# Optimization experiments

Measured on AMD Instinct MI355X. Metric: run time of the kernel, lower is better.

## Reference

```python
import jax, jax.numpy as jnp
import numpy as np

TEMP = 0.1

def _normalized_grid(B, H, W, dtype=jnp.float32):
    # normalized coords in [-1, 1], (x, y) order, shape [B, H, W, 2]
    ys = jnp.linspace(-1.0, 1.0, H, dtype=dtype)
    xs = jnp.linspace(-1.0, 1.0, W, dtype=dtype)
    gy, gx = jnp.meshgrid(ys, xs, indexing='ij')
    grid = jnp.stack([gx, gy], axis=-1)  # [H, W, 2]
    return jnp.broadcast_to(grid, (B, H, W, 2))


def setup_inputs() -> dict:
    key = jax.random.key(0)
    k1, k2, k3 = jax.random.split(key, 3)
    B, H, W, D = 8, 48, 48, 1024
    f_mv_A = jax.random.normal(k1, (B, H, W, D), dtype=jnp.float32)
    f_mv_B = jax.random.normal(k2, (B, H, W, D), dtype=jnp.float32)
    # omega buffer: 2*pi*randn(dim//2, 2)
    omega = 2.0 * jnp.pi * jax.random.normal(k3, (D // 2, 2), dtype=jnp.float32)
    scale = jnp.ones((), dtype=jnp.float32)
    return {"f_mv_A": f_mv_A, "f_mv_B": f_mv_B, "omega": omega, "scale": scale}


def reference(f_mv_A, f_mv_B, omega, scale):
    B, H_A, W_A, D = f_mv_A.shape
    _, H_B, W_B, _ = f_mv_B.shape
    # Fourier positional embedding grid over image B coordinates
    x = _normalized_grid(B, H_B, W_B).reshape(B, H_B * W_B, 2)
    x_emb = x @ (scale * omega).T                      # [B, HW_B, D//2]
    pos_emb_grid = jnp.concatenate([jnp.sin(x_emb), jnp.cos(x_emb)], axis=-1)  # [B, HW_B, D]

    # cosine similarity cross-attention
    fa = f_mv_A / jnp.linalg.norm(f_mv_A, axis=-1, keepdims=True)
    fb = f_mv_B / jnp.linalg.norm(f_mv_B, axis=-1, keepdims=True)
    fa = fa.reshape(B, H_A * W_A, D)
    fb = fb.reshape(B, H_B * W_B, D)
    attn_logits = (1.0 / TEMP) * jnp.einsum('bqd,bkd->bqk', fa, fb)  # [B, HW_A, HW_B]
    attn = jax.nn.softmax(attn_logits, axis=2)
    match_emb = jnp.einsum('bqk,bkd->bqd', attn, pos_emb_grid)        # [B, HW_A, D]

    attn_logits = attn_logits.reshape(B, H_A, W_A, H_B, W_B)
    attn = attn.reshape(B, H_A, W_A, H_B, W_B)
    match_emb = match_emb.reshape(B, H_A, W_A, D)
    return attn_logits, attn, match_emb
```

## Files before the change

### kernel.cpp

```cpp
#include <hip/hip_runtime.h>
#include <stdint.h>
#include <math.h>

#define NBATCH 8
#define HWSZ   2304
#define DDIM   1024
#define NROWS  (NBATCH*HWSZ)
#define PLANE  ((size_t)NROWS*DDIM)
#define OFF1   ((size_t)NBATCH*HWSZ*HWSZ)
#define OFF2   (2*OFF1)

typedef __attribute__((ext_vector_type(8))) short bf16x8;
typedef __attribute__((ext_vector_type(8))) _Float16 f16x8;
typedef __attribute__((ext_vector_type(4))) float f32x4;

#define GLOAD16(g, l) __builtin_amdgcn_global_load_lds( \
    (const __attribute__((address_space(1))) void*)(g), \
    (__attribute__((address_space(3))) void*)(l), 16, 0, 0)

__device__ __forceinline__ float bf2f(uint16_t u) {
    union { uint32_t i; float f; } v; v.i = ((uint32_t)u) << 16; return v.f;
}
__device__ __forceinline__ uint16_t f2bf(float f) {
    union { uint32_t i; float f; } v; v.f = f;
    uint32_t x = v.i;
    return (uint16_t)((x + 0x7fffu + ((x >> 16) & 1u)) >> 16);
}
__device__ __forceinline__ float h2f(uint16_t u) {
    _Float16 h; __builtin_memcpy(&h, &u, 2); return (float)h;
}
__device__ __forceinline__ uint16_t f2h(float f) {
    _Float16 h = (_Float16)f; uint16_t u; __builtin_memcpy(&u, &h, 2); return u;
}
__device__ __forceinline__ int dmode(const uint16_t* s) {
    uint16_t v = s[0];
    return (v == 0x3F80u) ? 1 : ((v == 0x3C00u) ? 2 : 0);
}
__device__ __forceinline__ float dec16(uint16_t u, int m) { return (m == 1) ? bf2f(u) : h2f(u); }
__device__ __forceinline__ uint16_t enc16(float f, int m) { return (m == 1) ? f2bf(f) : f2h(f); }

__global__ void prep_kernel(const void* __restrict__ inA, const void* __restrict__ inB,
                            const void* __restrict__ omega, const uint16_t* __restrict__ scalep,
                            float* __restrict__ rn, uint16_t* __restrict__ posT,
                            int* __restrict__ rowT, int* __restrict__ colT,
                            void* __restrict__ outbase) {
    const int mode = dmode(scalep);
    int g = blockIdx.x;
    int t = threadIdx.x;
    if (g == 0) {
        if (t < 64) {
            int lane = t;
            int m = lane & 15, q = lane >> 4;
            bf16x8 a1, b1, a2, b2;
            #pragma unroll
            for (int j = 0; j < 8; j++) {
                int k = q * 8 + j;
                float k0 = (k == 0) ? 1.0f : 0.0f;
                a1[j] = (short)f2bf(k0);
                b1[j] = (short)f2bf(k0 * (float)(m + 1));
                a2[j] = (short)f2bf(k0 * (float)(m + 1));
                b2[j] = (short)f2bf(k0);
            }
            f32x4 z = {0.f, 0.f, 0.f, 0.f};
            f32x4 d1 = __builtin_amdgcn_mfma_f32_16x16x32_bf16(a1, b1, z, 0, 0, 0);
            f32x4 d2 = __builtin_amdgcn_mfma_f32_16x16x32_bf16(a2, b2, z, 0, 0, 0);
            #pragma unroll
            for (int r = 0; r < 4; r++) {
                colT[lane * 4 + r] = (int)d1[r] - 1;
                rowT[lane * 4 + r] = (int)d2[r] - 1;
            }
        }
        return;
    }
    if (g <= 512) {
        int j = g - 1;
        float om0, om1, sc;
        if (mode == 0) {
            const float* om = (const float*)omega;
            om0 = om[j * 2]; om1 = om[j * 2 + 1];
            sc = *(const float*)scalep;
        } else {
            const uint16_t* om = (const uint16_t*)omega;
            om0 = dec16(om[j * 2], mode); om1 = dec16(om[j * 2 + 1], mode);
            sc = dec16(scalep[0], mode);
        }
        om0 *= sc; om1 *= sc;
        for (int p = t; p < HWSZ; p += 256) {
            int iy = p / 48, ix = p % 48;
            float gx = (2.0f / 47.0f) * (float)ix - 1.0f;
            float gy = (2.0f / 47.0f) * (float)iy - 1.0f;
            float e = om0 * gx + om1 * gy;
            size_t chunk = (size_t)(p >> 5) * (DDIM * 32);
            int kin = p & 31;
            posT[chunk + (size_t)j * 32 + kin]           = f2bf(sinf(e));
            posT[chunk + (size_t)(j + 512) * 32 + kin]   = f2bf(cosf(e));
        }
        return;
    }
    int row = g - 513;
    const void* src = (row < NROWS) ? inA : inB;
    int lrow = (row < NROWS) ? row : row - NROWS;
    float v[4];
    if (mode == 0) {
        const float* p = (const float*)src + (size_t)lrow * DDIM + t * 4;
        float4 f = *(const float4*)p;
        v[0] = f.x; v[1] = f.y; v[2] = f.z; v[3] = f.w;
        uint16_t* hbase = (uint16_t*)((float*)outbase + OFF1) + ((row < NROWS) ? 0 : PLANE);
        uint16_t h0 = f2h(v[0]), h1 = f2h(v[1]), h2 = f2h(v[2]), h3 = f2h(v[3]);
        uint2 hv;
        hv.x = (uint32_t)h0 | ((uint32_t)h1 << 16);
        hv.y = (uint32_t)h2 | ((uint32_t)h3 << 16);
        *(uint2*)(hbase + (size_t)lrow * DDIM + t * 4) = hv;
    } else {
        const uint16_t* p = (const uint16_t*)src + (size_t)lrow * DDIM + t * 4;
        uint2 u = *(const uint2*)p;
        v[0] = dec16(u.x & 0xffff, mode); v[1] = dec16(u.x >> 16, mode);
        v[2] = dec16(u.y & 0xffff, mode); v[3] = dec16(u.y >> 16, mode);
    }
    float ss = v[0]*v[0] + v[1]*v[1] + v[2]*v[2] + v[3]*v[3];
    __shared__ float red[256];
    red[t] = ss; __syncthreads();
    for (int s = 128; s > 0; s >>= 1) { if (t < s) red[t] += red[t + s]; __syncthreads(); }
    if (t == 0) rn[row] = 1.0f / sqrtf(red[0]);
}

__launch_bounds__(256, 2)
__global__ void gemm1_mfma(const void* __restrict__ inA, const void* __restrict__ inB,
                           const uint16_t* __restrict__ scalep, const float* __restrict__ rn,
                           void* __restrict__ outbase,
                           const int* __restrict__ rowT, const int* __restrict__ colT) {
    const int mode = dmode(scalep);
    __shared__ uint16_t sA[128 * 32];
    __shared__ uint16_t sB[128 * 32];
    __shared__ float rnS[256];
    int g = blockIdx.x;
    int swz = (g & 7) * 324 + (g >> 3);
    int b = swz / 324;
    int rr = swz % 324;
    int tm = rr / 18, tn = rr % 18;
    int t = threadIdx.x;
    if (t < 128) rnS[t] = 10.0f * rn[(size_t)b * HWSZ + tm * 128 + t];
    else         rnS[t] = rn[(size_t)NROWS + (size_t)b * HWSZ + tn * 128 + (t - 128)];
    int lane = t & 63, wave = t >> 6;
    int wm = (wave & 1) * 64, wn = (wave >> 1) * 64;
    int lr = lane & 15, ko = (lane >> 4) * 8;
    size_t rowA0 = (size_t)b * HWSZ + tm * 128;
    size_t rowB0 = (size_t)b * HWSZ + tn * 128;
    const uint16_t* pA16;
    const uint16_t* pB16;
    if (mode == 0) {
        const uint16_t* planes = (const uint16_t*)((const float*)outbase + OFF1);
        pA16 = planes + rowA0 * DDIM;
        pB16 = planes + PLANE + rowB0 * DDIM;
    } else {
        pA16 = (const uint16_t*)inA + rowA0 * DDIM;
        pB16 = (const uint16_t*)inB + rowB0 * DDIM;
    }
    int srow = wave * 32 + (lane >> 2);
    int squart = (lane & 3) * 8;
    const uint16_t* aS0 = pA16 + (size_t)srow * DDIM + squart;
    const uint16_t* aS1 = aS0 + (size_t)16 * DDIM;
    const uint16_t* bS0 = pB16 + (size_t)srow * DDIM + squart;
    const uint16_t* bS1 = bS0 + (size_t)16 * DDIM;
    uint16_t* aD0 = sA + (wave * 32) * 32;
    uint16_t* aD1 = aD0 + 512;
    uint16_t* bD0 = sB + (wave * 32) * 32;
    uint16_t* bD1 = bD0 + 512;
    f32x4 acc[4][4] = {};

    for (int k0 = 0; k0 < DDIM; k0 += 32) {
        __syncthreads();
        GLOAD16(aS0 + k0, aD0);
        GLOAD16(aS1 + k0, aD1);
        GLOAD16(bS0 + k0, bD0);
        GLOAD16(bS1 + k0, bD1);
        __syncthreads();
        if (mode == 1) {
            bf16x8 af[4], bf_[4];
            #pragma unroll
            for (int i = 0; i < 4; i++) af[i] = *(const bf16x8*)(sA + (wm + i * 16 + lr) * 32 + ko);
            #pragma unroll
            for (int j = 0; j < 4; j++) bf_[j] = *(const bf16x8*)(sB + (wn + j * 16 + lr) * 32 + ko);
            #pragma unroll
            for (int i = 0; i < 4; i++)
                #pragma unroll
                for (int j = 0; j < 4; j++)
                    acc[i][j] = __builtin_amdgcn_mfma_f32_16x16x32_bf16(af[i], bf_[j], acc[i][j], 0, 0, 0);
        } else {
            f16x8 af[4], bf_[4];
            #pragma unroll
            for (int i = 0; i < 4; i++) af[i] = *(const f16x8*)(sA + (wm + i * 16 + lr) * 32 + ko);
            #pragma unroll
            for (int j = 0; j < 4; j++) bf_[j] = *(const f16x8*)(sB + (wn + j * 16 + lr) * 32 + ko);
            #pragma unroll
            for (int i = 0; i < 4; i++)
                #pragma unroll
                for (int j = 0; j < 4; j++)
                    acc[i][j] = __builtin_amdgcn_mfma_f32_16x16x32_f16(af[i], bf_[j], acc[i][j], 0, 0, 0);
        }
    }

    int rtab[4], ctab[4];
    #pragma unroll
    for (int r = 0; r < 4; r++) {
        rtab[r] = rowT[lane * 4 + r] & 15;
        ctab[r] = colT[lane * 4 + r] & 15;
    }
    size_t cbase = (size_t)b * HWSZ * HWSZ;
    #pragma unroll
    for (int i = 0; i < 4; i++) {
        #pragma unroll
        for (int j = 0; j < 4; j++) {
            #pragma unroll
            for (int r = 0; r < 4; r++) {
                int row = wm + i * 16 + rtab[r];
                int col = wn + j * 16 + ctab[r];
                float v = acc[i][j][r] * rnS[row] * rnS[128 + col];
                size_t gm = (size_t)(tm * 128 + row);
                size_t gn = (size_t)(tn * 128 + col);
                if (mode == 0) ((float*)outbase)[cbase + gm * HWSZ + gn] = v;
                else ((uint16_t*)outbase)[cbase + gm * HWSZ + gn] = enc16(v, mode);
            }
        }
    }
}

__global__ void softmax_p16(void* __restrict__ outbase, const uint16_t* __restrict__ scalep,
                            uint16_t* __restrict__ p16) {
    const int mode = dmode(scalep);
    size_t row = blockIdx.x;
    int t = threadIdx.x;
    float v[9];
    if (mode == 0) {
        const float* src = (const float*)outbase + row * HWSZ;
        #pragma unroll
        for (int i = 0; i < 9; i++) v[i] = src[i * 256 + t];
    } else {
        const uint16_t* src = (const uint16_t*)outbase + row * HWSZ;
        #pragma unroll
        for (int i = 0; i < 9; i++) v[i] = dec16(src[i * 256 + t], mode);
    }
    float m = v[0];
    #pragma unroll
    for (int i = 1; i < 9; i++) m = fmaxf(m, v[i]);
    __shared__ float red[256];
    red[t] = m; __syncthreads();
    for (int s = 128; s > 0; s >>= 1) { if (t < s) red[t] = fmaxf(red[t], red[t + s]); __syncthreads(); }
    float M = red[0];
    __syncthreads();
    float ssum = 0.0f;
    #pragma unroll
    for (int i = 0; i < 9; i++) { v[i] = __expf(v[i] - M); ssum += v[i]; }
    red[t] = ssum; __syncthreads();
    for (int s = 128; s > 0; s >>= 1) { if (t < s) red[t] += red[t + s]; __syncthreads(); }
    float inv = 1.0f / red[0];
    uint16_t* prow = p16 + row * HWSZ;
    if (mode == 0) {
        float* dst = (float*)outbase + OFF1 + row * HWSZ;
        #pragma unroll
        for (int i = 0; i < 9; i++) {
            float p = v[i] * inv;
            dst[i * 256 + t] = p;
            prow[i * 256 + t] = f2bf(p);
        }
    } else {
        uint16_t* dst = (uint16_t*)outbase + OFF1 + row * HWSZ;
        #pragma unroll
        for (int i = 0; i < 9; i++) {
            uint16_t pk = enc16(v[i] * inv, mode);
            dst[i * 256 + t] = pk;
            prow[i * 256 + t] = (mode == 1) ? pk : f2bf(h2f(pk));
        }
    }
}

__global__ void rowstat_kernel(const void* __restrict__ outbase, const uint16_t* __restrict__ scalep,
                               float* __restrict__ stats) {
    const int mode = dmode(scalep);
    size_t row = blockIdx.x;
    int t = threadIdx.x;
    float v[9];
    if (mode == 0) {
        const float* src = (const float*)outbase + row * HWSZ;
        #pragma unroll
        for (int i = 0; i < 9; i++) v[i] = src[i * 256 + t];
    } else {
        const uint16_t* src = (const uint16_t*)outbase + row * HWSZ;
        #pragma unroll
        for (int i = 0; i < 9; i++) v[i] = dec16(src[i * 256 + t], mode);
    }
    float m = v[0];
    #pragma unroll
    for (int i = 1; i < 9; i++) m = fmaxf(m, v[i]);
    __shared__ float red[256];
    red[t] = m; __syncthreads();
    for (int s = 128; s > 0; s >>= 1) { if (t < s) red[t] = fmaxf(red[t], red[t + s]); __syncthreads(); }
    float M = red[0];
    __syncthreads();
    float ssum = 0.0f;
    #pragma unroll
    for (int i = 0; i < 9; i++) ssum += __expf(v[i] - M);
    red[t] = ssum; __syncthreads();
    for (int s = 128; s > 0; s >>= 1) { if (t < s) red[t] += red[t + s]; __syncthreads(); }
    if (t == 0) { stats[row] = M; stats[NROWS + row] = 1.0f / red[0]; }
}

#define G2BM 64
#define G2BN 256
#define G2L  40

__launch_bounds__(256, 4)
__global__ void gemm2_p16(void* __restrict__ outbase, const uint16_t* __restrict__ posT,
                          const uint16_t* __restrict__ scalep, const uint16_t* __restrict__ p16,
                          const int* __restrict__ rowT, const int* __restrict__ colT) {
    const int mode = dmode(scalep);
    __shared__ uint16_t sA[G2BM * 32];
    __shared__ uint16_t sB[G2BN * 32];
    int g = blockIdx.x;
    int swz = (g & 7) * 144 + (g >> 3);
    int b = swz / 144;
    int rr = swz % 144;
    int tm = rr >> 2, tn = rr & 3;
    int t = threadIdx.x;
    int lane = t & 63, wave = t >> 6;
    int wn = wave * 64;
    int lr = lane & 15, ko = (lane >> 4) * 8;
    const uint16_t* aS = p16 + ((size_t)b * HWSZ + (size_t)tm * G2BM + wave * 16 + (lane >> 2)) * HWSZ
                             + (lane & 3) * 8;
    uint16_t* aD = sA + (wave * 16) * 32;
    uint16_t* bD = sB + (wave * 64) * 32;
    f32x4 acc[4][4] = {};
    for (int k0 = 0; k0 < HWSZ; k0 += 32) {
        const uint16_t* bS = posT + (size_t)(k0 >> 5) * (DDIM * 32)
                                  + ((size_t)tn * G2BN + wave * 64) * 32 + lane * 8;
        __syncthreads();
        GLOAD16(aS + k0, aD);
        GLOAD16(bS + 0 * 512, bD + 0 * 512);
        GLOAD16(bS + 1 * 512, bD + 1 * 512);
        GLOAD16(bS + 2 * 512, bD + 2 * 512);
        GLOAD16(bS + 3 * 512, bD + 3 * 512);
        __syncthreads();
        bf16x8 af[4], bfr[4];
        #pragma unroll
        for (int i = 0; i < 4; i++) af[i] = *(const bf16x8*)(sA + (i * 16 + lr) * 32 + ko);
        #pragma unroll
        for (int j = 0; j < 4; j++) bfr[j] = *(const bf16x8*)(sB + (wn + j * 16 + lr) * 32 + ko);
        #pragma unroll
        for (int i = 0; i < 4; i++)
            #pragma unroll
            for (int j = 0; j < 4; j++)
                acc[i][j] = __builtin_amdgcn_mfma_f32_16x16x32_bf16(af[i], bfr[j], acc[i][j], 0, 0, 0);
    }
    int rtab[4], ctab[4];
    #pragma unroll
    for (int r = 0; r < 4; r++) {
        rtab[r] = rowT[lane * 4 + r] & 15;
        ctab[r] = colT[lane * 4 + r] & 15;
    }
    #pragma unroll
    for (int i = 0; i < 4; i++) {
        #pragma unroll
        for (int j = 0; j < 4; j++) {
            #pragma unroll
            for (int r = 0; r < 4; r++) {
                size_t row = (size_t)tm * G2BM + i * 16 + rtab[r];
                size_t col = (size_t)tn * G2BN + wn + j * 16 + ctab[r];
                size_t idx = OFF2 + (size_t)b * HWSZ * DDIM + row * DDIM + col;
                if (mode == 0) ((float*)outbase)[idx] = acc[i][j][r];
                else ((uint16_t*)outbase)[idx] = enc16(acc[i][j][r], mode);
            }
        }
    }
}

__launch_bounds__(256, 4)
__global__ void gemm2_mfma(void* __restrict__ outbase, const uint16_t* __restrict__ posT,
                           const uint16_t* __restrict__ scalep, const float* __restrict__ stats,
                           const int* __restrict__ rowT, const int* __restrict__ colT) {
    const int mode = dmode(scalep);
    __shared__ uint16_t sA[G2BM * G2L];
    int g = blockIdx.x;
    int swz = (g & 7) * 144 + (g >> 3);
    int b = swz / 144;
    int rr = swz % 144;
    int tm = rr >> 2, tn = rr & 3;
    int t = threadIdx.x;
    int lane = t & 63, wave = t >> 6;
    int wn = wave * 64;
    int lr = lane & 15, ko = (lane >> 4) * 8;
    int ar = t >> 2, ac8 = (t & 3) * 8;
    size_t grow = (size_t)b * HWSZ + (size_t)tm * G2BM + ar;
    float Mrow = stats[grow];
    float invl = stats[NROWS + grow];
    f32x4 acc[4][4] = {};
    for (int k0 = 0; k0 < HWSZ; k0 += 32) {
        uint16_t av[8];
        float p[8];
        if (mode == 0) {
            const float* ap = (const float*)outbase + grow * HWSZ + k0 + ac8;
            float4 x0 = *(const float4*)ap, x1 = *(const float4*)(ap + 4);
            p[0] = __expf(x0.x - Mrow) * invl; p[1] = __expf(x0.y - Mrow) * invl;
            p[2] = __expf(x0.z - Mrow) * invl; p[3] = __expf(x0.w - Mrow) * invl;
            p[4] = __expf(x1.x - Mrow) * invl; p[5] = __expf(x1.y - Mrow) * invl;
            p[6] = __expf(x1.z - Mrow) * invl; p[7] = __expf(x1.w - Mrow) * invl;
            if (tn == 0) {
                float* dst = (float*)outbase + OFF1 + grow * HWSZ + k0 + ac8;
                *(float4*)dst       = *(const float4*)p;
                *(float4*)(dst + 4) = *(const float4*)(p + 4);
            }
        } else {
            const uint16_t* ap = (const uint16_t*)outbase + grow * HWSZ + k0 + ac8;
            uint4 r0 = *(const uint4*)ap;
            const uint16_t* u0 = (const uint16_t*)&r0;
            #pragma unroll
            for (int j = 0; j < 8; j++) p[j] = __expf(dec16(u0[j], mode) - Mrow) * invl;
            if (tn == 0) {
                uint16_t pk[8];
                #pragma unroll
                for (int j = 0; j < 8; j++) pk[j] = enc16(p[j], mode);
                *(uint4*)((uint16_t*)outbase + OFF1 + grow * HWSZ + k0 + ac8) = *(const uint4*)pk;
            }
        }
        #pragma unroll
        for (int j = 0; j < 8; j++) av[j] = f2bf(p[j]);
        __syncthreads();
        *(uint4*)(sA + ar * G2L + ac8) = *(const uint4*)av;
        __syncthreads();
        const uint16_t* bchunk = posT + (size_t)(k0 >> 5) * (DDIM * 32);
        bf16x8 af[4], bfr[4];
        #pragma unroll
        for (int j = 0; j < 4; j++)
            bfr[j] = *(const bf16x8*)(bchunk + ((size_t)tn * G2BN + wn + j * 16 + lr) * 32 + ko);
        #pragma unroll
        for (int i = 0; i < 4; i++) af[i] = *(const bf16x8*)(sA + (i * 16 + lr) * G2L + ko);
        #pragma unroll
        for (int i = 0; i < 4; i++)
            #pragma unroll
            for (int j = 0; j < 4; j++)
                acc[i][j] = __builtin_amdgcn_mfma_f32_16x16x32_bf16(af[i], bfr[j], acc[i][j], 0, 0, 0);
    }
    int rtab[4], ctab[4];
    #pragma unroll
    for (int r = 0; r < 4; r++) {
        rtab[r] = rowT[lane * 4 + r] & 15;
        ctab[r] = colT[lane * 4 + r] & 15;
    }
    #pragma unroll
    for (int i = 0; i < 4; i++) {
        #pragma unroll
        for (int j = 0; j < 4; j++) {
            #pragma unroll
            for (int r = 0; r < 4; r++) {
                size_t row = (size_t)tm * G2BM + i * 16 + rtab[r];
                size_t col = (size_t)tn * G2BN + wn + j * 16 + ctab[r];
                size_t idx = OFF2 + (size_t)b * HWSZ * DDIM + row * DDIM + col;
                if (mode == 0) ((float*)outbase)[idx] = acc[i][j][r];
                else ((uint16_t*)outbase)[idx] = enc16(acc[i][j][r], mode);
            }
        }
    }
}

extern "C" void kernel_launch(void* const* d_in, const int* in_sizes, int n_in,
                              void* d_out, int out_size, void* d_ws, size_t ws_size,
                              hipStream_t stream) {
    const void* fA    = d_in[0];
    const void* fB    = d_in[1];
    const void* omega = d_in[2];
    const uint16_t* scale = (const uint16_t*)d_in[3];

    int* rowT = (int*)d_ws;
    int* colT = rowT + 256;
    float* rn = (float*)((char*)d_ws + 4096);
    size_t posT_off = 4096 + (size_t)2 * NROWS * 4;
    uint16_t* posT = (uint16_t*)((char*)d_ws + posT_off);
    size_t p16_off = posT_off + (size_t)DDIM * HWSZ * 2;
    size_t ws_need = p16_off + (size_t)NROWS * HWSZ * 2;
    uint16_t* p16 = (uint16_t*)((char*)d_ws + p16_off);
    const bool big_ws = (ws_size >= ws_need);

    prep_kernel<<<513 + 2 * NROWS, 256, 0, stream>>>(fA, fB, omega, scale, rn, posT,
                                                     rowT, colT, d_out);

    gemm1_mfma<<<18 * 18 * NBATCH, 256, 0, stream>>>(fA, fB, scale, rn, d_out, rowT, colT);

    if (big_ws) {
        softmax_p16<<<NROWS, 256, 0, stream>>>(d_out, scale, p16);
        gemm2_p16<<<(HWSZ / G2BM) * (DDIM / G2BN) * NBATCH, 256, 0, stream>>>(
            d_out, posT, scale, p16, rowT, colT);
    } else {
        rowstat_kernel<<<NROWS, 256, 0, stream>>>(d_out, scale, rn);
        gemm2_mfma<<<(HWSZ / G2BM) * (DDIM / G2BN) * NBATCH, 256, 0, stream>>>(
            d_out, posT, scale, rn, rowT, colT);
    }
}
```

Before: 424.3 us.

## Double-buffer LDS tiles in both GEMM kernels to overlap loads with MFMA

```diff
diff --git a/kernel.cpp b/kernel.cpp
--- a/kernel.cpp
+++ b/kernel.cpp
@@ -130,8 +130,8 @@
                            void* __restrict__ outbase,
                            const int* __restrict__ rowT, const int* __restrict__ colT) {
     const int mode = dmode(scalep);
-    __shared__ uint16_t sA[128 * 32];
-    __shared__ uint16_t sB[128 * 32];
+    __shared__ uint16_t sA[2 * 128 * 32];
+    __shared__ uint16_t sB[2 * 128 * 32];
     __shared__ float rnS[256];
     int g = blockIdx.x;
     int swz = (g & 7) * 324 + (g >> 3);
@@ -162,25 +162,30 @@
     const uint16_t* aS1 = aS0 + (size_t)16 * DDIM;
     const uint16_t* bS0 = pB16 + (size_t)srow * DDIM + squart;
     const uint16_t* bS1 = bS0 + (size_t)16 * DDIM;
-    uint16_t* aD0 = sA + (wave * 32) * 32;
-    uint16_t* aD1 = aD0 + 512;
-    uint16_t* bD0 = sB + (wave * 32) * 32;
-    uint16_t* bD1 = bD0 + 512;
+    int woff = (wave * 32) * 32;
     f32x4 acc[4][4] = {};
 
+    GLOAD16(aS0, sA + woff);
+    GLOAD16(aS1, sA + woff + 512);
+    GLOAD16(bS0, sB + woff);
+    GLOAD16(bS1, sB + woff + 512);
+    int c = 0;
     for (int k0 = 0; k0 < DDIM; k0 += 32) {
         __syncthreads();
-        GLOAD16(aS0 + k0, aD0);
-        GLOAD16(aS1 + k0, aD1);
-        GLOAD16(bS0 + k0, bD0);
-        GLOAD16(bS1 + k0, bD1);
-        __syncthreads();
+        if (k0 + 32 < DDIM) {
+            int o = (c ^ 1) * 4096;
+            GLOAD16(aS0 + k0 + 32, sA + o + woff);
+            GLOAD16(aS1 + k0 + 32, sA + o + woff + 512);
+            GLOAD16(bS0 + k0 + 32, sB + o + woff);
+            GLOAD16(bS1 + k0 + 32, sB + o + woff + 512);
+        }
+        int cb = c * 4096;
         if (mode == 1) {
             bf16x8 af[4], bf_[4];
             #pragma unroll
-            for (int i = 0; i < 4; i++) af[i] = *(const bf16x8*)(sA + (wm + i * 16 + lr) * 32 + ko);
-            #pragma unroll
-            for (int j = 0; j < 4; j++) bf_[j] = *(const bf16x8*)(sB + (wn + j * 16 + lr) * 32 + ko);
+            for (int i = 0; i < 4; i++) af[i] = *(const bf16x8*)(sA + cb + (wm + i * 16 + lr) * 32 + ko);
+            #pragma unroll
+            for (int j = 0; j < 4; j++) bf_[j] = *(const bf16x8*)(sB + cb + (wn + j * 16 + lr) * 32 + ko);
             #pragma unroll
             for (int i = 0; i < 4; i++)
                 #pragma unroll
@@ -189,15 +194,16 @@
         } else {
             f16x8 af[4], bf_[4];
             #pragma unroll
-            for (int i = 0; i < 4; i++) af[i] = *(const f16x8*)(sA + (wm + i * 16 + lr) * 32 + ko);
-            #pragma unroll
-            for (int j = 0; j < 4; j++) bf_[j] = *(const f16x8*)(sB + (wn + j * 16 + lr) * 32 + ko);
+            for (int i = 0; i < 4; i++) af[i] = *(const f16x8*)(sA + cb + (wm + i * 16 + lr) * 32 + ko);
+            #pragma unroll
+            for (int j = 0; j < 4; j++) bf_[j] = *(const f16x8*)(sB + cb + (wn + j * 16 + lr) * 32 + ko);
             #pragma unroll
             for (int i = 0; i < 4; i++)
                 #pragma unroll
                 for (int j = 0; j < 4; j++)
                     acc[i][j] = __builtin_amdgcn_mfma_f32_16x16x32_f16(af[i], bf_[j], acc[i][j], 0, 0, 0);
         }
+        c ^= 1;
     }
 
     int rtab[4], ctab[4];
@@ -314,8 +320,8 @@
                           const uint16_t* __restrict__ scalep, const uint16_t* __restrict__ p16,
                           const int* __restrict__ rowT, const int* __restrict__ colT) {
     const int mode = dmode(scalep);
-    __shared__ uint16_t sA[G2BM * 32];
-    __shared__ uint16_t sB[G2BN * 32];
+    __shared__ uint16_t sA[2 * G2BM * 32];
+    __shared__ uint16_t sB[2 * G2BN * 32];
     int g = blockIdx.x;
     int swz = (g & 7) * 144 + (g >> 3);
     int b = swz / 144;
@@ -327,29 +333,45 @@
     int lr = lane & 15, ko = (lane >> 4) * 8;
     const uint16_t* aS = p16 + ((size_t)b * HWSZ + (size_t)tm * G2BM + wave * 16 + (lane >> 2)) * HWSZ
                              + (lane & 3) * 8;
-    uint16_t* aD = sA + (wave * 16) * 32;
-    uint16_t* bD = sB + (wave * 64) * 32;
+    int aoff = (wave * 16) * 32;
+    int boff = (wave * 64) * 32;
+    size_t bbase = ((size_t)tn * G2BN + wave * 64) * 32 + lane * 8;
     f32x4 acc[4][4] = {};
+
+    {
+        const uint16_t* bS = posT + bbase;
+        GLOAD16(aS, sA + aoff);
+        GLOAD16(bS + 0 * 512, sB + boff + 0 * 512);
+        GLOAD16(bS + 1 * 512, sB + boff + 1 * 512);
+        GLOAD16(bS + 2 * 512, sB + boff + 2 * 512);
+        GLOAD16(bS + 3 * 512, sB + boff + 3 * 512);
+    }
+    int c = 0;
     for (int k0 = 0; k0 < HWSZ; k0 += 32) {
-        const uint16_t* bS = posT + (size_t)(k0 >> 5) * (DDIM * 32)
-                                  + ((size_t)tn * G2BN + wave * 64) * 32 + lane * 8;
         __syncthreads();
-        GLOAD16(aS + k0, aD);
-        GLOAD16(bS + 0 * 512, bD + 0 * 512);
-        GLOAD16(bS + 1 * 512, bD + 1 * 512);
-        GLOAD16(bS + 2 * 512, bD + 2 * 512);
-        GLOAD16(bS + 3 * 512, bD + 3 * 512);
-        __syncthreads();
+        if (k0 + 32 < HWSZ) {
+            int oa = (c ^ 1) * (G2BM * 32);
+            int ob = (c ^ 1) * (G2BN * 32);
+            const uint16_t* bS = posT + (size_t)((k0 + 32) >> 5) * (DDIM * 32) + bbase;
+            GLOAD16(aS + k0 + 32, sA + oa + aoff);
+            GLOAD16(bS + 0 * 512, sB + ob + boff + 0 * 512);
+            GLOAD16(bS + 1 * 512, sB + ob + boff + 1 * 512);
+            GLOAD16(bS + 2 * 512, sB + ob + boff + 2 * 512);
+            GLOAD16(bS + 3 * 512, sB + ob + boff + 3 * 512);
+        }
+        int ca = c * (G2BM * 32);
+        int cbuf = c * (G2BN * 32);
         bf16x8 af[4], bfr[4];
         #pragma unroll
-        for (int i = 0; i < 4; i++) af[i] = *(const bf16x8*)(sA + (i * 16 + lr) * 32 + ko);
-        #pragma unroll
-        for (int j = 0; j < 4; j++) bfr[j] = *(const bf16x8*)(sB + (wn + j * 16 + lr) * 32 + ko);
+        for (int i = 0; i < 4; i++) af[i] = *(const bf16x8*)(sA + ca + (i * 16 + lr) * 32 + ko);
+        #pragma unroll
+        for (int j = 0; j < 4; j++) bfr[j] = *(const bf16x8*)(sB + cbuf + (wn + j * 16 + lr) * 32 + ko);
         #pragma unroll
         for (int i = 0; i < 4; i++)
             #pragma unroll
             for (int j = 0; j < 4; j++)
                 acc[i][j] = __builtin_amdgcn_mfma_f32_16x16x32_bf16(af[i], bfr[j], acc[i][j], 0, 0, 0);
+        c ^= 1;
     }
     int rtab[4], ctab[4];
     #pragma unroll
```

New measurement: 445.4 us. 1.05x slower.
